# Optimization experiments

Hardware: AMD Instinct MI355X
Metric: run time of the kernel (lower is better)

The kernel has to match this reference:

```python
import jax, jax.numpy as jnp
import numpy as np

D = 28 * 28  # 784


def setup_inputs() -> dict:
    key = jax.random.key(0)
    k1, k2, k3 = jax.random.split(key, 3)
    x = jax.random.normal(k1, (128, 28, 28), dtype=jnp.float32)
    W = jax.random.normal(k2, (D + D * D, 10), dtype=jnp.float32) * 0.01
    b = jax.random.normal(k3, (10,), dtype=jnp.float32) * 0.01
    return {"x": x, "W": W, "b": b}


def reference(x, W, b):
    # x: [B, 28, 28] -> x1: [B, 784]
    x1 = x.reshape(-1, D)
    # Faithful to the torch module: materialize the batched outer product
    # x2[b,i,j] = x1[b,i] * x1[b,j]  -> [B, 784, 784]
    x2 = x1[:, :, None] * x1[:, None, :]
    feats = jnp.concatenate([x1, x2.reshape(-1, D * D)], axis=1)  # [B, 615440]
    return feats @ W + b  # [B, 10]
```

## Files before the change

kernel.cpp:

```cpp
#include <hip/hip_runtime.h>
#include <hip/hip_bf16.h>
#include <cstdint>
#include <cstddef>


typedef short short8 __attribute__((ext_vector_type(8)));
typedef float f32x4 __attribute__((ext_vector_type(4)));

#define NB   128
#define DD   784
#define NC   10
#define KCH  112
#define NKC  7
#define IG   16
#define NG   49
#define NBLK (NG*NKC)
#define LDK  136
#define LDKU 68
#define PSTRIDE 352

__device__ __forceinline__ uint32_t f2bfbits(float f) {
  uint32_t u = __builtin_bit_cast(uint32_t, f);
  u += 0x7FFFu + ((u >> 16) & 1u);
  return u >> 16;
}

template <int ATOMIC>
__global__ __launch_bounds__(512, 4)
void bilinear_main(const float* __restrict__ x, const float* __restrict__ W,
                   const float* __restrict__ bias, float* __restrict__ P,
                   float* __restrict__ out) {
  __shared__ unsigned short ldsW[160 * LDK];
  uint32_t* lds32 = (uint32_t*)ldsW;

  const int tid  = threadIdx.x;
  const int blk  = blockIdx.x;
  const int g    = blk / NKC;
  const int kc   = blk - g * NKC;
  const int i0   = g * IG;
  const int lane = tid & 63;
  const int w    = tid >> 6;
  const int wm   = w >> 2;
  const int bq2  = w & 3;
  const int l15  = lane & 15;
  const int q    = lane >> 4;
  const int jbase = kc * KCH;

  {
    const float* w2base = W + 7840 + (size_t)i0 * 7840 + (size_t)jbase * NC;
    #pragma unroll
    for (int half = 0; half < 2; ++half) {
      const int gi = half * 512 + tid;
      if (gi < 896) {
        const int il = gi / 56;
        const int k  = gi - il * 56;
        const float* p = w2base + il * 7840 + k * 20;
        const float4 a0 = ((const float4*)p)[0];
        const float4 a1 = ((const float4*)p)[1];
        const float4 a2 = ((const float4*)p)[2];
        const float4 a3 = ((const float4*)p)[3];
        const float4 a4 = ((const float4*)p)[4];
        const float v[20] = {a0.x,a0.y,a0.z,a0.w, a1.x,a1.y,a1.z,a1.w,
                             a2.x,a2.y,a2.z,a2.w, a3.x,a3.y,a3.z,a3.w,
                             a4.x,a4.y,a4.z,a4.w};
        #pragma unroll
        for (int c = 0; c < 10; ++c) {
          const uint32_t lo = f2bfbits(v[c]);
          const uint32_t hi = f2bfbits(v[c + 10]);
          lds32[(c * 16 + il) * LDKU + k] = lo | (hi << 16);
        }
      }
    }
    for (int idx = tid; idx < 160 * 8; idx += 512) {
      const int row  = idx >> 3;
      const int colu = idx & 7;
      lds32[row * LDKU + 56 + colu] = 0;
    }
  }

  short8 bq[2][4];
  #pragma unroll
  for (int bg = 0; bg < 2; ++bg) {
    const int b = bq2 * 32 + bg * 16 + l15;
    const float* xrow = x + (size_t)b * DD + jbase;
    #pragma unroll
    for (int ks = 0; ks < 4; ++ks) {
      const int jloc = ks * 32 + q * 8;
      float v[8];
      if (jloc < KCH) {
        const float4 p0 = *(const float4*)(xrow + jloc);
        const float4 p1 = *(const float4*)(xrow + jloc + 4);
        v[0] = p0.x; v[1] = p0.y; v[2] = p0.z; v[3] = p0.w;
        v[4] = p1.x; v[5] = p1.y; v[6] = p1.z; v[7] = p1.w;
      } else {
        #pragma unroll
        for (int e = 0; e < 8; ++e) v[e] = 0.f;
      }
      short8 s;
      #pragma unroll
      for (int e = 0; e < 8; ++e) s[e] = (short)f2bfbits(v[e]);
      bq[bg][ks] = s;
    }
  }

  float xv[2][4];
  #pragma unroll
  for (int bg = 0; bg < 2; ++bg) {
    const int b = bq2 * 32 + bg * 16 + l15;
    #pragma unroll
    for (int r = 0; r < 4; ++r)
      xv[bg][r] = x[(size_t)b * DD + i0 + q * 4 + r];
  }

  __syncthreads();

  float yacc[2][5] = {};
  const int tbase = wm * 5;
  #pragma unroll
  for (int t = 0; t < 5; ++t) {
    const int tile = tbase + t;
    f32x4 acc[2] = {};
    const unsigned short* arow = &ldsW[(tile * 16 + l15) * LDK + q * 8];
    #pragma unroll
    for (int ks = 0; ks < 4; ++ks) {
      const short8 a = *(const short8*)(arow + ks * 32);
      #pragma unroll
      for (int bg = 0; bg < 2; ++bg)
        acc[bg] = __builtin_amdgcn_mfma_f32_16x16x32_bf16(a, bq[bg][ks], acc[bg], 0, 0, 0);
    }
    #pragma unroll
    for (int r = 0; r < 4; ++r) {
      float w1 = 0.f;
      if (kc == 0) w1 = W[(i0 + q * 4 + r) * NC + tile];
      #pragma unroll
      for (int bg = 0; bg < 2; ++bg)
        yacc[bg][t] += xv[bg][r] * (acc[bg][r] + w1);
    }
  }

  #pragma unroll
  for (int bg = 0; bg < 2; ++bg) {
    #pragma unroll
    for (int t = 0; t < 5; ++t) {
      float v = yacc[bg][t];
      v += __shfl_down(v, 16);
      v += __shfl_down(v, 32);
      if (q == 0) {
        const int bc = (bq2 * 32 + bg * 16 + l15) * NC + tbase + t;
        if constexpr (ATOMIC == 0) {
          P[(size_t)bc * PSTRIDE + blk] = v;
        } else {
          if (blk == 0) v += bias[tbase + t];
          atomicAdd(&out[bc], v);
        }
      }
    }
  }
}

__global__ __launch_bounds__(64)
void reduce_partials(const float* __restrict__ P, const float* __restrict__ bias,
                     float* __restrict__ out) {
  const int bc = blockIdx.x;
  const int l  = threadIdx.x;
  float s = 0.f;
  for (int k = l; k < NBLK; k += 64) s += P[(size_t)bc * PSTRIDE + k];
  #pragma unroll
  for (int off = 32; off; off >>= 1) s += __shfl_down(s, off);
  if (l == 0) out[bc] = s + bias[bc % NC];
}

extern "C" void kernel_launch(void* const* d_in, const int* in_sizes, int n_in,
                              void* d_out, int out_size, void* d_ws, size_t ws_size,
                              hipStream_t stream) {
  const float* x    = (const float*)d_in[0];
  const float* W    = (const float*)d_in[1];
  const float* bias = (const float*)d_in[2];
  float* out = (float*)d_out;
  float* P   = (float*)d_ws;

  const size_t need = (size_t)NB * NC * PSTRIDE * sizeof(float);
  if (ws_size >= need) {
    bilinear_main<0><<<NBLK, 512, 0, stream>>>(x, W, bias, P, out);
    reduce_partials<<<NB * NC, 64, 0, stream>>>(P, bias, out);
  } else {
    hipMemsetAsync(d_out, 0, (size_t)NB * NC * sizeof(float), stream);
    bilinear_main<1><<<NBLK, 512, 0, stream>>>(x, W, bias, P, out);
  }
}
```

Baseline: 22.50 us.

## Transpose partials layout to block-major and reduce with vectorized tree kernel

Partial sums are now stored block-major, so each main-kernel block writes contiguous outputs and the reduction reads float4 columns across blocks. The reduce kernel handles four outputs per 512-thread block using wave shuffles plus LDS, cutting the reduce grid from 1280 blocks to 320. The xv load also becomes a single float4 load. Strided reads across blocks in the reduce may coalesce worse, but each thread now does one load instead of a loop.

```diff
diff --git a/kernel.cpp b/kernel.cpp
--- a/kernel.cpp
+++ b/kernel.cpp
@@ -17,7 +17,7 @@
 #define NBLK (NG*NKC)
 #define LDK  136
 #define LDKU 68
-#define PSTRIDE 352
+#define NOUT (NB*NC)
 
 __device__ __forceinline__ uint32_t f2bfbits(float f) {
   uint32_t u = __builtin_bit_cast(uint32_t, f);
@@ -107,9 +107,8 @@
   #pragma unroll
   for (int bg = 0; bg < 2; ++bg) {
     const int b = bq2 * 32 + bg * 16 + l15;
-    #pragma unroll
-    for (int r = 0; r < 4; ++r)
-      xv[bg][r] = x[(size_t)b * DD + i0 + q * 4 + r];
+    const float4 xq = *(const float4*)(x + (size_t)b * DD + i0 + q * 4);
+    xv[bg][0] = xq.x; xv[bg][1] = xq.y; xv[bg][2] = xq.z; xv[bg][3] = xq.w;
   }
 
   __syncthreads();
@@ -146,28 +145,52 @@
       v += __shfl_down(v, 16);
       v += __shfl_down(v, 32);
       if (q == 0) {
-        const int bc = (bq2 * 32 + bg * 16 + l15) * NC + tbase + t;
+        const int b = bq2 * 32 + bg * 16 + l15;
         if constexpr (ATOMIC == 0) {
-          P[(size_t)bc * PSTRIDE + blk] = v;
+          P[(size_t)blk * NOUT + b * NC + tbase + t] = v;
         } else {
-          if (blk == 0) v += bias[tbase + t];
-          atomicAdd(&out[bc], v);
+          float vv = v;
+          if (blk == 0) vv += bias[tbase + t];
+          atomicAdd(&out[b * NC + tbase + t], vv);
         }
       }
     }
   }
 }
 
-__global__ __launch_bounds__(64)
-void reduce_partials(const float* __restrict__ P, const float* __restrict__ bias,
-                     float* __restrict__ out) {
-  const int bc = blockIdx.x;
-  const int l  = threadIdx.x;
-  float s = 0.f;
-  for (int k = l; k < NBLK; k += 64) s += P[(size_t)bc * PSTRIDE + k];
-  #pragma unroll
-  for (int off = 32; off; off >>= 1) s += __shfl_down(s, off);
-  if (l == 0) out[bc] = s + bias[bc % NC];
+__global__ __launch_bounds__(512)
+void reduce_tree(const float* __restrict__ P, const float* __restrict__ bias,
+                 float* __restrict__ out) {
+  __shared__ float red[8][4];
+  const int f = blockIdx.x;
+  const int t = threadIdx.x;
+  const int w = t >> 6, l = t & 63;
+
+  float4 v = make_float4(0.f, 0.f, 0.f, 0.f);
+  if (t < NBLK) v = ((const float4*)P)[(size_t)t * (NOUT / 4) + f];
+
+  #pragma unroll
+  for (int off = 32; off; off >>= 1) {
+    v.x += __shfl_down(v.x, off);
+    v.y += __shfl_down(v.y, off);
+    v.z += __shfl_down(v.z, off);
+    v.w += __shfl_down(v.w, off);
+  }
+  if (l == 0) { red[w][0] = v.x; red[w][1] = v.y; red[w][2] = v.z; red[w][3] = v.w; }
+  __syncthreads();
+  if (t == 0) {
+    float4 s = make_float4(0.f, 0.f, 0.f, 0.f);
+    #pragma unroll
+    for (int k = 0; k < 8; ++k) {
+      s.x += red[k][0]; s.y += red[k][1]; s.z += red[k][2]; s.w += red[k][3];
+    }
+    const int bc = f * 4;
+    s.x += bias[bc % NC];
+    s.y += bias[(bc + 1) % NC];
+    s.z += bias[(bc + 2) % NC];
+    s.w += bias[(bc + 3) % NC];
+    *(float4*)&out[bc] = s;
+  }
 }
 
 extern "C" void kernel_launch(void* const* d_in, const int* in_sizes, int n_in,
@@ -179,12 +202,12 @@
   float* out = (float*)d_out;
   float* P   = (float*)d_ws;
 
-  const size_t need = (size_t)NB * NC * PSTRIDE * sizeof(float);
+  const size_t need = (size_t)NBLK * NOUT * sizeof(float);
   if (ws_size >= need) {
     bilinear_main<0><<<NBLK, 512, 0, stream>>>(x, W, bias, P, out);
-    reduce_partials<<<NB * NC, 64, 0, stream>>>(P, bias, out);
+    reduce_tree<<<NOUT / 4, 512, 0, stream>>>(P, bias, out);
   } else {
-    hipMemsetAsync(d_out, 0, (size_t)NB * NC * sizeof(float), stream);
+    hipMemsetAsync(d_out, 0, (size_t)NOUT * sizeof(float), stream);
     bilinear_main<1><<<NBLK, 512, 0, stream>>>(x, W, bias, P, out);
   }
 }
```

Result: no change. 22.34 us (-0.7%).
